# Kernel tuning notes

Measured on AMD Instinct MI355X. Metric: run time of the kernel, lower is better.

Reference implementation:

```python
import jax, jax.numpy as jnp
import numpy as np

C = 0.001          # hyperbolic curvature
SEG_LEN = 50       # L // segments = 1000 // 20
N_SEG = 20
EPS_BN = 1e-5


def _log0(x, c):
    # Poincare-ball log map at origin: artanh(sqrt(c)||x||)/(sqrt(c)||x||) * x
    sc = jnp.sqrt(c)
    n = jnp.linalg.norm(x, axis=1, keepdims=True)
    sn = jnp.clip(sc * n, 1e-12, 1.0 - 1e-5)
    return (jnp.arctanh(sn) / sn) * x


def _exp0(v, c):
    # Poincare-ball exp map at origin: tanh(sqrt(c)||v||)/(sqrt(c)||v||) * v
    sc = jnp.sqrt(c)
    n = jnp.linalg.norm(v, axis=1, keepdims=True)
    sn = jnp.maximum(sc * n, 1e-12)
    return (jnp.tanh(sn) / sn) * v


def _bn(h, g, b):
    # BatchNorm1d in training mode: biased batch statistics
    mu = h.mean(axis=0)
    var = h.var(axis=0)
    return g * (h - mu) * jax.lax.rsqrt(var + EPS_BN) + b


def setup_inputs() -> dict:
    key = jax.random.key(0)
    ks = jax.random.split(key, 12)
    B, D_IN, D_H, D_OUT = 32768, 784, 256, 10
    x = jax.random.normal(ks[0], (B, D_IN), dtype=jnp.float32)
    W1 = jax.random.normal(ks[1], (D_IN, D_H), dtype=jnp.float32) * 0.03
    b1 = jnp.zeros((D_H,), dtype=jnp.float32)
    g1 = jnp.ones((D_H,), dtype=jnp.float32)
    be1 = jnp.zeros((D_H,), dtype=jnp.float32)
    # filters near unit magnitude so H**50 stays bounded
    Hr = 1.0 + 0.01 * jax.random.normal(ks[2], (N_SEG, D_H), dtype=jnp.float32)
    Hi = 0.01 * jax.random.normal(ks[3], (N_SEG, D_H), dtype=jnp.float32)
    alphas = 1.0 + 0.05 * jax.random.normal(ks[4], (N_SEG,), dtype=jnp.float32)
    betas = 0.05 * jax.random.normal(ks[5], (N_SEG,), dtype=jnp.float32)
    g2 = jnp.ones((D_H,), dtype=jnp.float32)
    be2 = jnp.zeros((D_H,), dtype=jnp.float32)
    W2 = jax.random.normal(ks[6], (D_H, D_OUT), dtype=jnp.float32) * 0.06
    b2 = jnp.zeros((D_OUT,), dtype=jnp.float32)
    return {"x": x, "W1": W1, "b1": b1, "g1": g1, "be1": be1,
            "Hr": Hr, "Hi": Hi, "alphas": alphas, "betas": betas,
            "g2": g2, "be2": be2, "W2": W2, "b2": b2}


def reference(x, W1, b1, g1, be1, Hr, Hi, alphas, betas, g2, be2, W2, b2):
    h = jax.nn.relu(_bn(x @ W1 + b1, g1, be1))  # [B, D_H]

    def step(h, p):
        hr, hi, a, bt = p
        u = _log0(h, C)
        U = jnp.fft.fft(u, axis=1)                      # [B, D_H] complex
        H_eff = jax.lax.complex(hr, hi) ** SEG_LEN      # [D_H] complex
        v = jnp.real(jnp.fft.ifft(U * H_eff[None, :], axis=1))
        y = _exp0(v, C)
        return a * y + bt * h, None

    h, _ = jax.lax.scan(step, h, (Hr, Hi, alphas, betas))
    h = jax.nn.relu(_bn(h, g2, be2))
    return h @ W2 + b2
```

## Files before the change

kernel.cpp:

```cpp
#include <hip/hip_runtime.h>
#include <math.h>

#define NB     32768
#define DH     256
#define DIN    784
#define DOUT   10
#define NSEG   20
#define EPSBN  1e-5f
#define SCRT   0.031622776601683794f
#define PI_D   3.14159265358979323846

typedef _Float16 h16;
typedef _Float16 f16x8 __attribute__((ext_vector_type(8)));
typedef float    f32x4 __attribute__((ext_vector_type(4)));

__device__ __forceinline__ void gl_lds16(const void* g, void* l){
  __builtin_amdgcn_global_load_lds(
      (const __attribute__((address_space(1))) unsigned int*)g,
      (__attribute__((address_space(3))) unsigned int*)l, 16, 0, 0);
}
__device__ __forceinline__ void stageB32K(const char* src, char* ldsbase, int wid, int lane){
  #pragma unroll
  for (int q = 0; q < 8; ++q)
    gl_lds16(src + wid*8192 + q*1024 + lane*16, ldsbase + wid*8192 + q*1024);
}

__device__ __forceinline__ float2 cmul(float2 a, float2 b) {
    return make_float2(fmaf(a.x, b.x, -(a.y*b.y)), fmaf(a.x, b.y, a.y*b.x));
}
__device__ __forceinline__ float2 cadd(float2 a, float2 b){ return make_float2(a.x+b.x, a.y+b.y); }
__device__ __forceinline__ float2 csub(float2 a, float2 b){ return make_float2(a.x-b.x, a.y-b.y); }
__device__ __forceinline__ int physi(int i){ return i ^ ((i >> 4) & 15); }

__global__ void prep_G(const float* __restrict__ Hr, const float* __restrict__ Hi,
                       float2* __restrict__ Gt, float* __restrict__ st1, float* __restrict__ st2)
{
  __shared__ double HrE[256], HiE[256];
  int k = threadIdx.x, s = blockIdx.x;
  double ar = (double)Hr[s*256 + k], ai = (double)Hi[s*256 + k];
  double pr = 1.0, pi = 0.0;
  for (int i = 0; i < 50; ++i){ double nr = pr*ar - pi*ai; pi = pr*ai + pi*ar; pr = nr; }
  HrE[k] = pr; HiE[k] = pi;
  if (s == 0){ st1[k] = 0.f; st1[256+k] = 0.f; st2[k] = 0.f; st2[256+k] = 0.f; }
  __syncthreads();
  int km = (256 - k) & 255;
  float gr = (float)(0.5 * (HrE[k] + HrE[km]));
  float gi = (float)(0.5 * (HiE[k] - HiE[km]));
  Gt[s*256 + k] = make_float2(gr, gi);
}

__global__ void prep_packW(const float* __restrict__ W1, char* __restrict__ wsW)
{
  int blk = blockIdx.x; int ch = blk >> 1, lo = blk & 1;
  int n = threadIdx.x;
  char* out = wsW + (size_t)ch*32768 + lo*16384;
  int xr = (n & 3) << 4;
  #pragma unroll
  for (int j = 0; j < 32; ++j){
    int w  = 2*j;
    int k2 = (w ^ xr) >> 1;
    int k  = ch*32 + k2;
    float v = (k < 784) ? W1[(size_t)k*256 + n] : 0.f;
    h16 hv = (h16)v;
    h16 ov = lo ? (h16)(v - (float)hv) : hv;
    *(h16*)(out + n*64 + w) = ov;
  }
}

__global__ __launch_bounds__(256) void gemm1_mfma(const float* __restrict__ x,
                                                  const char* __restrict__ wsW,
                                                  float* __restrict__ t)
{
  __shared__ __attribute__((aligned(16))) char BB[2][32768];
  __shared__ __attribute__((aligned(16))) char AB[2][8192];
  const int tid = threadIdx.x;
  const int lane = tid & 63, wid = tid >> 6;
  const int cl = lane & 15, g4 = lane >> 4;
  const int brow = blockIdx.x * 64;
  const int nb0 = wid * 64;
  const int arow = tid & 63, kq = tid >> 6;

  f32x4 zz = {0.f,0.f,0.f,0.f};
  f32x4 acc[4][4];
  #pragma unroll
  for (int i = 0; i < 4; ++i)
    #pragma unroll
    for (int j = 0; j < 4; ++j) acc[i][j] = zz;

  float4 a0, a1;
  const float4 z4 = make_float4(0.f,0.f,0.f,0.f);

  stageB32K(wsW, BB[0], wid, lane);
  {
    int k0 = kq*8;
    const float* p = x + (size_t)(brow + arow)*784 + k0;
    a0 = *(const float4*)p; a1 = *(const float4*)(p + 4);
    f16x8 hv, lv;
    float vv[8] = {a0.x,a0.y,a0.z,a0.w,a1.x,a1.y,a1.z,a1.w};
    #pragma unroll
    for (int j = 0; j < 8; ++j){ h16 hh = (h16)vv[j]; hv[j] = hh; lv[j] = (h16)(vv[j] - (float)hh); }
    int aoff = arow*64 + 16*(kq ^ (arow & 3));
    *(f16x8*)(AB[0] + aoff) = hv;
    *(f16x8*)(AB[0] + 4096 + aoff) = lv;
  }
  __syncthreads();

  int cur = 0;
  for (int ch = 0; ch < 25; ++ch){
    float4 n0 = z4, n1 = z4;
    bool have_next = (ch < 24);
    if (have_next){
      stageB32K(wsW + (size_t)(ch+1)*32768, BB[cur^1], wid, lane);
      int k0 = (ch+1)*32 + kq*8;
      if (k0 + 7 < 784){
        const float* p = x + (size_t)(brow + arow)*784 + k0;
        n0 = *(const float4*)p; n1 = *(const float4*)(p + 4);
      }
    }
    const char* Bc = BB[cur];
    const char* Ac = AB[cur];
    f16x8 bh[4], bl[4], ah[4], al[4];
    #pragma unroll
    for (int ni = 0; ni < 4; ++ni){
      int n = nb0 + ni*16 + cl;
      int boff = n*64 + 16*(g4 ^ (n & 3));
      bh[ni] = *(const f16x8*)(Bc + boff);
      bl[ni] = *(const f16x8*)(Bc + 16384 + boff);
    }
    #pragma unroll
    for (int mi = 0; mi < 4; ++mi){
      int row = mi*16 + cl;
      int aoff = row*64 + 16*(g4 ^ (row & 3));
      ah[mi] = *(const f16x8*)(Ac + aoff);
      al[mi] = *(const f16x8*)(Ac + 4096 + aoff);
    }
    #pragma unroll
    for (int mi = 0; mi < 4; ++mi)
      #pragma unroll
      for (int ni = 0; ni < 4; ++ni){
        acc[mi][ni] = __builtin_amdgcn_mfma_f32_16x16x32_f16(ah[mi], bh[ni], acc[mi][ni], 0,0,0);
        acc[mi][ni] = __builtin_amdgcn_mfma_f32_16x16x32_f16(al[mi], bh[ni], acc[mi][ni], 0,0,0);
        acc[mi][ni] = __builtin_amdgcn_mfma_f32_16x16x32_f16(ah[mi], bl[ni], acc[mi][ni], 0,0,0);
      }
    if (have_next){
      f16x8 hv, lv;
      float vv[8] = {n0.x,n0.y,n0.z,n0.w,n1.x,n1.y,n1.z,n1.w};
      #pragma unroll
      for (int j = 0; j < 8; ++j){ h16 hh = (h16)vv[j]; hv[j] = hh; lv[j] = (h16)(vv[j] - (float)hh); }
      int aoff = arow*64 + 16*(kq ^ (arow & 3));
      *(f16x8*)(AB[cur^1] + aoff) = hv;
      *(f16x8*)(AB[cur^1] + 4096 + aoff) = lv;
      __syncthreads();
      cur ^= 1;
    }
  }
  #pragma unroll
  for (int mi = 0; mi < 4; ++mi)
    #pragma unroll
    for (int ni = 0; ni < 4; ++ni)
      #pragma unroll
      for (int r = 0; r < 4; ++r){
        int row = brow + mi*16 + g4*4 + r;
        int col = nb0 + ni*16 + cl;
        t[(size_t)row*256 + col] = acc[mi][ni][r];
      }
}

__global__ __launch_bounds__(256) void colstats_kernel(const float* __restrict__ t,
                                                       float* __restrict__ sum,
                                                       float* __restrict__ ssq)
{
  const int col = threadIdx.x;
  float s = 0.f, q = 0.f;
  for (int r = blockIdx.x; r < NB; r += gridDim.x){
    float v = t[(size_t)r * DH + col];
    s += v; q = fmaf(v, v, q);
  }
  atomicAdd(&sum[col], s);
  atomicAdd(&ssq[col], q);
}

__global__ void finalize_kernel(float* __restrict__ st)
{
  int j = threadIdx.x;
  float mu = st[j] * (1.f/(float)NB);
  float var = st[DH+j] * (1.f/(float)NB) - mu*mu;
  st[j] = mu;
  st[DH+j] = rsqrtf(var + EPSBN);
}

template<bool FWD>
__device__ __forceinline__ void fft_stage0(const float2 X[4], float2* dst, int lane, float wc, float ws)
{
    float2 a=X[0], b=X[1], c=X[2], d=X[3];
    float2 t0 = cadd(a,c), t1 = csub(a,c), t2 = cadd(b,d), bd = csub(b,d);
    float2 t3 = FWD ? make_float2(bd.y, -bd.x) : make_float2(-bd.y, bd.x);
    float2 w1 = make_float2(wc, FWD ? -ws : ws);
    float2 w2 = cmul(w1,w1);
    float2 w3 = cmul(w2,w1);
    int j = lane << 2;
    dst[physi(j)]   = cadd(t0,t2);
    dst[physi(j+1)] = cmul(cadd(t1,t3), w1);
    dst[physi(j+2)] = cmul(csub(t0,t2), w2);
    dst[physi(j+3)] = cmul(csub(t1,t3), w3);
}

template<int TT, bool FWD>
__device__ __forceinline__ void fft_stage_lds(const float2* src, float2* dst, int lane, float wc, float ws)
{
    const int s_ = 1 << (2*TT);
    int i = lane;
    float2 a = src[physi(i)];
    float2 b = src[physi(i+64)];
    float2 c = src[physi(i+128)];
    float2 d = src[physi(i+192)];
    float2 t0 = cadd(a,c), t1 = csub(a,c), t2 = cadd(b,d), bd = csub(b,d);
    float2 t3 = FWD ? make_float2(bd.y, -bd.x) : make_float2(-bd.y, bd.x);
    float2 w1 = make_float2(wc, FWD ? -ws : ws);
    float2 w2 = cmul(w1,w1);
    float2 w3 = cmul(w2,w1);
    int j = i + 3*(i & ~(s_-1));
    dst[physi(j)]      = cadd(t0,t2);
    dst[physi(j+s_)]   = cmul(cadd(t1,t3), w1);
    dst[physi(j+2*s_)] = cmul(csub(t0,t2), w2);
    dst[physi(j+3*s_)] = cmul(csub(t1,t3), w3);
}

template<bool FWD>
__device__ __forceinline__ void fft_stage3(const float2* src, float2 X[4], int lane)
{
    float2 a = src[physi(lane)];
    float2 b = src[physi(lane+64)];
    float2 c = src[physi(lane+128)];
    float2 d = src[physi(lane+192)];
    float2 t0 = cadd(a,c), t1 = csub(a,c), t2 = cadd(b,d), bd = csub(b,d);
    float2 t3 = FWD ? make_float2(bd.y, -bd.x) : make_float2(-bd.y, bd.x);
    X[0] = cadd(t0,t2);
    X[1] = cadd(t1,t3);
    X[2] = csub(t0,t2);
    X[3] = csub(t1,t3);
}

__global__ __launch_bounds__(256) void seg_fft(
    float* __restrict__ t, const float2* __restrict__ Gt,
    const float* __restrict__ st1,
    const float* __restrict__ g1, const float* __restrict__ be1,
    const float* __restrict__ alphas, const float* __restrict__ betas)
{
  __shared__ float2 bufA[4][256];
  __shared__ float2 bufB[4][256];
  const int lane = threadIdx.x & 63;
  const int wid  = threadIdx.x >> 6;
  const int row  = (blockIdx.x << 2) | wid;
  float2* A  = bufA[wid];
  float2* Bb = bufB[wid];

  float c0,s0,c1,s1,c2,s2;
  {
    const float k = 6.283185307179586f / 256.f;
    sincosf(k * (float)lane,          &s0, &c0);
    sincosf(k * (float)(lane & ~3),   &s1, &c1);
    sincosf(k * (float)(lane & ~15),  &s2, &c2);
  }

  float2 X[4];
  #pragma unroll
  for (int j = 0; j < 4; ++j) {
    int col = lane + 64*j;
    float v = t[(size_t)row * DH + col];
    v = g1[col] * (v - st1[col]) * st1[DH + col] + be1[col];
    X[j] = make_float2(fmaxf(v, 0.f), 0.f);
  }

  fft_stage0<true>(X, A, lane, c0, s0);
  fft_stage_lds<1,true>(A, Bb, lane, c1, s1);
  fft_stage_lds<2,true>(Bb, A, lane, c2, s2);
  fft_stage3<true>(A, X, lane);

  for (int sg = 0; sg < NSEG; ++sg) {
    const float2* Gp = Gt + sg*256;
    float2 g[4];
    #pragma unroll
    for (int r = 0; r < 4; ++r) g[r] = Gp[lane + 64*r];

    float p1 = 0.f, p2 = 0.f;
    #pragma unroll
    for (int r = 0; r < 4; ++r) {
      float m  = fmaf(X[r].x, X[r].x, X[r].y * X[r].y);
      float g2 = fmaf(g[r].x, g[r].x, g[r].y * g[r].y);
      p1 += m;
      p2 = fmaf(m, g2, p2);
    }
    #pragma unroll
    for (int m = 32; m > 0; m >>= 1) {
      p1 += __shfl_xor(p1, m, 64);
      p2 += __shfl_xor(p2, m, 64);
    }
    float nh  = sqrtf(p1 * (1.f/256.f));
    float snh = fminf(fmaxf(SCRT*nh, 1e-12f), 1.f - 1e-5f);
    float lam = atanhf(snh) / snh;
    float nv  = lam * sqrtf(p2 * (1.f/256.f));
    float snv = fmaxf(SCRT*nv, 1e-12f);
    float muv = tanhf(snv) / snv;
    float sc  = alphas[sg] * muv * lam;
    float bt  = betas[sg];
    #pragma unroll
    for (int r = 0; r < 4; ++r) {
      float Ar = fmaf(sc, g[r].x, bt);
      float Bi = sc * g[r].y;
      float xr = X[r].x, xi = X[r].y;
      X[r].x = fmaf(xr, Ar, -(xi*Bi));
      X[r].y = fmaf(xr, Bi,  xi*Ar);
    }
  }

  fft_stage0<false>(X, A, lane, c0, s0);
  fft_stage_lds<1,false>(A, Bb, lane, c1, s1);
  fft_stage_lds<2,false>(Bb, A, lane, c2, s2);
  fft_stage3<false>(A, X, lane);

  #pragma unroll
  for (int j = 0; j < 4; ++j)
    t[(size_t)row * DH + lane + 64*j] = X[j].x * (1.f/256.f);
}

__global__ __launch_bounds__(256) void final_kernel(
    const float* __restrict__ t, const float* __restrict__ st2,
    const float* __restrict__ g2, const float* __restrict__ be2,
    const float* __restrict__ W2, const float* __restrict__ b2,
    float* __restrict__ out)
{
  __shared__ __attribute__((aligned(16))) float Hs[16][260];
  __shared__ float W2s[DH*DOUT];
  __shared__ float b2s[16];
  const int tid = threadIdx.x;
  for (int idx = tid; idx < DH*DOUT; idx += 256) W2s[idx] = W2[idx];
  if (tid < DOUT) b2s[tid] = b2[tid];
  const int r0 = blockIdx.x * 16;
  for (int idx = tid; idx < 16*(DH/4); idx += 256) {
    int r  = idx >> 6;
    int c4 = (idx & 63) << 2;
    float4 v = *(const float4*)&t[(size_t)(r0 + r)*DH + c4];
    float o[4] = {v.x, v.y, v.z, v.w};
    #pragma unroll
    for (int k = 0; k < 4; ++k) {
      int c = c4 + k;
      float w = g2[c] * (o[k] - st2[c]) * st2[DH+c] + be2[c];
      o[k] = fmaxf(w, 0.f);
    }
    *(float4*)&Hs[r][c4] = make_float4(o[0], o[1], o[2], o[3]);
  }
  __syncthreads();
  if (tid < 16*DOUT) {
    int r = tid / DOUT, j = tid - DOUT*r;
    float acc = b2s[j];
    for (int k = 0; k < DH; ++k)
      acc = fmaf(Hs[r][k], W2s[k*DOUT + j], acc);
    out[(size_t)(r0 + r)*DOUT + j] = acc;
  }
}

extern "C" void kernel_launch(void* const* d_in, const int* in_sizes, int n_in,
                              void* d_out, int out_size, void* d_ws, size_t ws_size,
                              hipStream_t stream) {
  const float* x      = (const float*)d_in[0];
  const float* W1     = (const float*)d_in[1];
  const float* g1     = (const float*)d_in[3];
  const float* be1    = (const float*)d_in[4];
  const float* Hr     = (const float*)d_in[5];
  const float* Hi     = (const float*)d_in[6];
  const float* alphas = (const float*)d_in[7];
  const float* betas  = (const float*)d_in[8];
  const float* g2     = (const float*)d_in[9];
  const float* be2    = (const float*)d_in[10];
  const float* W2     = (const float*)d_in[11];
  const float* b2     = (const float*)d_in[12];
  float* out = (float*)d_out;

  char* ws = (char*)d_ws;
  float*  t    = (float*)(ws);
  char*   wsW  = ws + 33554432;
  float*  st1  = (float*)(ws + 34373632);
  float*  st2  = (float*)(ws + 34375680);
  float2* Gt   = (float2*)(ws + 34377728);

  prep_G    <<<NSEG, 256, 0, stream>>>(Hr, Hi, Gt, st1, st2);
  prep_packW<<<50, 256, 0, stream>>>(W1, wsW);
  gemm1_mfma<<<NB/64, 256, 0, stream>>>(x, wsW, t);
  colstats_kernel<<<256, 256, 0, stream>>>(t, st1, st1 + DH);
  finalize_kernel<<<1, 256, 0, stream>>>(st1);
  seg_fft   <<<NB/4, 256, 0, stream>>>(t, Gt, st1, g1, be1, alphas, betas);
  colstats_kernel<<<256, 256, 0, stream>>>(t, st2, st2 + DH);
  finalize_kernel<<<1, 256, 0, stream>>>(st2);
  final_kernel<<<NB/16, 256, 0, stream>>>(t, st2, g2, be2, W2, b2, out);
}
```

Baseline: 561.6 us.

## Retile GEMM to 128-row blocks, precompute filter magnitudes, fuse reductions, use fast intrinsics

```diff
diff --git a/kernel.cpp b/kernel.cpp
--- a/kernel.cpp
+++ b/kernel.cpp
@@ -14,16 +14,16 @@
 typedef _Float16 f16x8 __attribute__((ext_vector_type(8)));
 typedef float    f32x4 __attribute__((ext_vector_type(4)));
 
+__device__ __forceinline__ float flog2(float x){ float r; asm("v_log_f32 %0, %1" : "=v"(r) : "v"(x)); return r; }
+__device__ __forceinline__ float fexp2(float x){ float r; asm("v_exp_f32 %0, %1" : "=v"(r) : "v"(x)); return r; }
+__device__ __forceinline__ float frcp (float x){ float r; asm("v_rcp_f32 %0, %1" : "=v"(r) : "v"(x)); return r; }
+__device__ __forceinline__ float fsqrt(float x){ float r; asm("v_sqrt_f32 %0, %1" : "=v"(r) : "v"(x)); return r; }
+
 __device__ __forceinline__ void gl_lds16(const void* g, void* l){
   __builtin_amdgcn_global_load_lds(
       (const __attribute__((address_space(1))) unsigned int*)g,
       (__attribute__((address_space(3))) unsigned int*)l, 16, 0, 0);
 }
-__device__ __forceinline__ void stageB32K(const char* src, char* ldsbase, int wid, int lane){
-  #pragma unroll
-  for (int q = 0; q < 8; ++q)
-    gl_lds16(src + wid*8192 + q*1024 + lane*16, ldsbase + wid*8192 + q*1024);
-}
 
 __device__ __forceinline__ float2 cmul(float2 a, float2 b) {
     return make_float2(fmaf(a.x, b.x, -(a.y*b.y)), fmaf(a.x, b.y, a.y*b.x));
@@ -33,7 +33,7 @@
 __device__ __forceinline__ int physi(int i){ return i ^ ((i >> 4) & 15); }
 
 __global__ void prep_G(const float* __restrict__ Hr, const float* __restrict__ Hi,
-                       float2* __restrict__ Gt, float* __restrict__ st1, float* __restrict__ st2)
+                       float4* __restrict__ Gq, float* __restrict__ st1, float* __restrict__ st2)
 {
   __shared__ double HrE[256], HiE[256];
   int k = threadIdx.x, s = blockIdx.x;
@@ -46,7 +46,7 @@
   int km = (256 - k) & 255;
   float gr = (float)(0.5 * (HrE[k] + HrE[km]));
   float gi = (float)(0.5 * (HiE[k] - HiE[km]));
-  Gt[s*256 + k] = make_float2(gr, gi);
+  Gq[s*256 + k] = make_float4(gr, gi, fmaf(gr, gr, gi*gi), 0.f);
 }
 
 __global__ void prep_packW(const float* __restrict__ W1, char* __restrict__ wsW)
@@ -67,101 +67,101 @@
   }
 }
 
-__global__ __launch_bounds__(256) void gemm1_mfma(const float* __restrict__ x,
+__global__ __launch_bounds__(512) void gemm1_mfma(const float* __restrict__ x,
                                                   const char* __restrict__ wsW,
                                                   float* __restrict__ t)
 {
+  __shared__ __attribute__((aligned(16))) char AB[2][16384];
   __shared__ __attribute__((aligned(16))) char BB[2][32768];
-  __shared__ __attribute__((aligned(16))) char AB[2][8192];
   const int tid = threadIdx.x;
   const int lane = tid & 63, wid = tid >> 6;
   const int cl = lane & 15, g4 = lane >> 4;
-  const int brow = blockIdx.x * 64;
-  const int nb0 = wid * 64;
-  const int arow = tid & 63, kq = tid >> 6;
-
-  f32x4 zz = {0.f,0.f,0.f,0.f};
-  f32x4 acc[4][4];
-  #pragma unroll
-  for (int i = 0; i < 4; ++i)
-    #pragma unroll
-    for (int j = 0; j < 4; ++j) acc[i][j] = zz;
-
-  float4 a0, a1;
+  const int wr = wid >> 1, wc = wid & 1;
+  const int brow = blockIdx.x * 128;
+  const int arow = tid >> 2, asl = tid & 3;
+  const int aoff = arow*64 + ((asl*16) ^ ((arow & 3) << 4));
+  const float* xrow = x + (size_t)(brow + arow)*784;
+
+  f32x4 acc[2][8];
+  #pragma unroll
+  for (int i = 0; i < 2; ++i)
+    #pragma unroll
+    for (int j = 0; j < 8; ++j) acc[i][j] = (f32x4){0.f,0.f,0.f,0.f};
+
   const float4 z4 = make_float4(0.f,0.f,0.f,0.f);
 
-  stageB32K(wsW, BB[0], wid, lane);
+  #pragma unroll
+  for (int q = 0; q < 4; ++q)
+    gl_lds16(wsW + q*8192 + wid*1024 + lane*16, &BB[0][0] + q*8192 + wid*1024);
   {
-    int k0 = kq*8;
-    const float* p = x + (size_t)(brow + arow)*784 + k0;
-    a0 = *(const float4*)p; a1 = *(const float4*)(p + 4);
+    const float* p = xrow + asl*8;
+    float4 a0 = *(const float4*)p, a1 = *(const float4*)(p + 4);
+    float vv[8] = {a0.x,a0.y,a0.z,a0.w,a1.x,a1.y,a1.z,a1.w};
     f16x8 hv, lv;
-    float vv[8] = {a0.x,a0.y,a0.z,a0.w,a1.x,a1.y,a1.z,a1.w};
     #pragma unroll
     for (int j = 0; j < 8; ++j){ h16 hh = (h16)vv[j]; hv[j] = hh; lv[j] = (h16)(vv[j] - (float)hh); }
-    int aoff = arow*64 + 16*(kq ^ (arow & 3));
-    *(f16x8*)(AB[0] + aoff) = hv;
-    *(f16x8*)(AB[0] + 4096 + aoff) = lv;
+    *(f16x8*)(&AB[0][0] + aoff) = hv;
+    *(f16x8*)(&AB[0][0] + 8192 + aoff) = lv;
   }
   __syncthreads();
 
   int cur = 0;
   for (int ch = 0; ch < 25; ++ch){
-    float4 n0 = z4, n1 = z4;
-    bool have_next = (ch < 24);
-    if (have_next){
-      stageB32K(wsW + (size_t)(ch+1)*32768, BB[cur^1], wid, lane);
-      int k0 = (ch+1)*32 + kq*8;
-      if (k0 + 7 < 784){
-        const float* p = x + (size_t)(brow + arow)*784 + k0;
-        n0 = *(const float4*)p; n1 = *(const float4*)(p + 4);
+    const bool hn = (ch < 24);
+    float4 na0 = z4, na1 = z4;
+    if (hn){
+      const char* src = wsW + (size_t)(ch+1)*32768;
+      #pragma unroll
+      for (int q = 0; q < 4; ++q)
+        gl_lds16(src + q*8192 + wid*1024 + lane*16, &BB[cur^1][0] + q*8192 + wid*1024);
+      int kg = (ch+1)*32 + asl*8;
+      if (kg < 784){
+        const float* p = xrow + kg;
+        na0 = *(const float4*)p; na1 = *(const float4*)(p + 4);
       }
     }
-    const char* Bc = BB[cur];
-    const char* Ac = AB[cur];
-    f16x8 bh[4], bl[4], ah[4], al[4];
-    #pragma unroll
-    for (int ni = 0; ni < 4; ++ni){
-      int n = nb0 + ni*16 + cl;
-      int boff = n*64 + 16*(g4 ^ (n & 3));
-      bh[ni] = *(const f16x8*)(Bc + boff);
-      bl[ni] = *(const f16x8*)(Bc + 16384 + boff);
-    }
-    #pragma unroll
-    for (int mi = 0; mi < 4; ++mi){
-      int row = mi*16 + cl;
-      int aoff = row*64 + 16*(g4 ^ (row & 3));
-      ah[mi] = *(const f16x8*)(Ac + aoff);
-      al[mi] = *(const f16x8*)(Ac + 4096 + aoff);
-    }
-    #pragma unroll
-    for (int mi = 0; mi < 4; ++mi)
+    const char* Ac = &AB[cur][0];
+    const char* Bc = &BB[cur][0];
+    f16x8 ah[2], al[2];
+    #pragma unroll
+    for (int mi = 0; mi < 2; ++mi){
+      int row = wr*32 + mi*16 + cl;
+      int off = row*64 + ((g4*16) ^ ((row & 3) << 4));
+      ah[mi] = *(const f16x8*)(Ac + off);
+      al[mi] = *(const f16x8*)(Ac + 8192 + off);
+    }
+    #pragma unroll
+    for (int ni = 0; ni < 8; ++ni){
+      int n = wc*128 + ni*16 + cl;
+      int boff = n*64 + ((g4*16) ^ ((n & 3) << 4));
+      f16x8 bh = *(const f16x8*)(Bc + boff);
+      f16x8 bl = *(const f16x8*)(Bc + 16384 + boff);
       #pragma unroll
-      for (int ni = 0; ni < 4; ++ni){
-        acc[mi][ni] = __builtin_amdgcn_mfma_f32_16x16x32_f16(ah[mi], bh[ni], acc[mi][ni], 0,0,0);
-        acc[mi][ni] = __builtin_amdgcn_mfma_f32_16x16x32_f16(al[mi], bh[ni], acc[mi][ni], 0,0,0);
-        acc[mi][ni] = __builtin_amdgcn_mfma_f32_16x16x32_f16(ah[mi], bl[ni], acc[mi][ni], 0,0,0);
+      for (int mi = 0; mi < 2; ++mi){
+        acc[mi][ni] = __builtin_amdgcn_mfma_f32_16x16x32_f16(ah[mi], bh, acc[mi][ni], 0,0,0);
+        acc[mi][ni] = __builtin_amdgcn_mfma_f32_16x16x32_f16(al[mi], bh, acc[mi][ni], 0,0,0);
+        acc[mi][ni] = __builtin_amdgcn_mfma_f32_16x16x32_f16(ah[mi], bl, acc[mi][ni], 0,0,0);
       }
-    if (have_next){
+    }
+    if (hn){
+      float vv[8] = {na0.x,na0.y,na0.z,na0.w,na1.x,na1.y,na1.z,na1.w};
       f16x8 hv, lv;
-      float vv[8] = {n0.x,n0.y,n0.z,n0.w,n1.x,n1.y,n1.z,n1.w};
       #pragma unroll
       for (int j = 0; j < 8; ++j){ h16 hh = (h16)vv[j]; hv[j] = hh; lv[j] = (h16)(vv[j] - (float)hh); }
-      int aoff = arow*64 + 16*(kq ^ (arow & 3));
-      *(f16x8*)(AB[cur^1] + aoff) = hv;
-      *(f16x8*)(AB[cur^1] + 4096 + aoff) = lv;
+      *(f16x8*)(&AB[cur^1][0] + aoff) = hv;
+      *(f16x8*)(&AB[cur^1][0] + 8192 + aoff) = lv;
       __syncthreads();
       cur ^= 1;
     }
   }
   #pragma unroll
-  for (int mi = 0; mi < 4; ++mi)
-    #pragma unroll
-    for (int ni = 0; ni < 4; ++ni)
+  for (int mi = 0; mi < 2; ++mi)
+    #pragma unroll
+    for (int ni = 0; ni < 8; ++ni)
       #pragma unroll
       for (int r = 0; r < 4; ++r){
-        int row = brow + mi*16 + g4*4 + r;
-        int col = nb0 + ni*16 + cl;
+        int row = brow + wr*32 + mi*16 + g4*4 + r;
+        int col = wc*128 + ni*16 + cl;
         t[(size_t)row*256 + col] = acc[mi][ni][r];
       }
 }
@@ -242,7 +242,7 @@
 }
 
 __global__ __launch_bounds__(256) void seg_fft(
-    float* __restrict__ t, const float2* __restrict__ Gt,
+    float* __restrict__ t, const float4* __restrict__ Gq,
     const float* __restrict__ st1,
     const float* __restrict__ g1, const float* __restrict__ be1,
     const float* __restrict__ alphas, const float* __restrict__ betas)
@@ -277,33 +277,39 @@
   fft_stage_lds<2,true>(Bb, A, lane, c2, s2);
   fft_stage3<true>(A, X, lane);
 
+  const int upper = lane & 32;
   for (int sg = 0; sg < NSEG; ++sg) {
-    const float2* Gp = Gt + sg*256;
-    float2 g[4];
+    const float4* Gp = Gq + sg*256;
+    float4 g[4];
     #pragma unroll
     for (int r = 0; r < 4; ++r) g[r] = Gp[lane + 64*r];
 
     float p1 = 0.f, p2 = 0.f;
     #pragma unroll
     for (int r = 0; r < 4; ++r) {
-      float m  = fmaf(X[r].x, X[r].x, X[r].y * X[r].y);
-      float g2 = fmaf(g[r].x, g[r].x, g[r].y * g[r].y);
+      float m = fmaf(X[r].x, X[r].x, X[r].y * X[r].y);
       p1 += m;
-      p2 = fmaf(m, g2, p2);
-    }
-    #pragma unroll
-    for (int m = 32; m > 0; m >>= 1) {
-      p1 += __shfl_xor(p1, m, 64);
-      p2 += __shfl_xor(p2, m, 64);
-    }
-    float nh  = sqrtf(p1 * (1.f/256.f));
-    float snh = fminf(fmaxf(SCRT*nh, 1e-12f), 1.f - 1e-5f);
-    float lam = atanhf(snh) / snh;
-    float nv  = lam * sqrtf(p2 * (1.f/256.f));
+      p2 = fmaf(m, g[r].z, p2);
+    }
+    float send = upper ? p1 : p2;
+    float recv = __shfl_xor(send, 32, 64);
+    float w = (upper ? p2 : p1) + recv;
+    #pragma unroll
+    for (int m = 1; m <= 16; m <<= 1) w += __shfl_xor(w, m, 64);
+    float wsw = __shfl_xor(w, 32, 64);
+    float P1 = upper ? wsw : w;
+    float P2 = upper ? w   : wsw;
+
+    float nh  = fsqrt(P1 * (1.f/256.f));
+    float sn  = fminf(fmaxf(SCRT*nh, 1e-12f), 1.f - 1e-5f);
+    float lam = 0.34657359028f * flog2((1.f+sn) * frcp(1.f-sn)) * frcp(sn);
+    float nv  = lam * fsqrt(P2 * (1.f/256.f));
     float snv = fmaxf(SCRT*nv, 1e-12f);
-    float muv = tanhf(snv) / snv;
+    float e   = fexp2(fminf(snv, 40.f) * 2.88539008178f);
+    float muv = (e - 1.f) * frcp((e + 1.f) * snv);
     float sc  = alphas[sg] * muv * lam;
     float bt  = betas[sg];
+
     #pragma unroll
     for (int r = 0; r < 4; ++r) {
       float Ar = fmaf(sc, g[r].x, bt);
@@ -382,15 +388,15 @@
   char*   wsW  = ws + 33554432;
   float*  st1  = (float*)(ws + 34373632);
   float*  st2  = (float*)(ws + 34375680);
-  float2* Gt   = (float2*)(ws + 34377728);
-
-  prep_G    <<<NSEG, 256, 0, stream>>>(Hr, Hi, Gt, st1, st2);
+  float4* Gq   = (float4*)(ws + 34377728);
+
+  prep_G    <<<NSEG, 256, 0, stream>>>(Hr, Hi, Gq, st1, st2);
   prep_packW<<<50, 256, 0, stream>>>(W1, wsW);
-  gemm1_mfma<<<NB/64, 256, 0, stream>>>(x, wsW, t);
-  colstats_kernel<<<256, 256, 0, stream>>>(t, st1, st1 + DH);
+  gemm1_mfma<<<NB/128, 512, 0, stream>>>(x, wsW, t);
+  colstats_kernel<<<2048, 256, 0, stream>>>(t, st1, st1 + DH);
   finalize_kernel<<<1, 256, 0, stream>>>(st1);
-  seg_fft   <<<NB/4, 256, 0, stream>>>(t, Gt, st1, g1, be1, alphas, betas);
-  colstats_kernel<<<256, 256, 0, stream>>>(t, st2, st2 + DH);
+  seg_fft   <<<NB/4, 256, 0, stream>>>(t, Gq, st1, g1, be1, alphas, betas);
+  colstats_kernel<<<2048, 256, 0, stream>>>(t, st2, st2 + DH);
   finalize_kernel<<<1, 256, 0, stream>>>(st2);
   final_kernel<<<NB/16, 256, 0, stream>>>(t, st2, g2, be2, W2, b2, out);
 }
```

Result: faster. 460.7 us (-18.0%).
